# Kernel optimization log

Hardware: AMD Instinct MI355X
Metric: run time of the kernel (lower is better)

## Reference

```python
import jax, jax.numpy as jnp
import numpy as np

D = H = W = 128
NUM_STEPS = 7  # MONAI DVF2DDF default


def _base_grid(dtype):
    zz, yy, xx = jnp.meshgrid(jnp.arange(D, dtype=dtype),
                              jnp.arange(H, dtype=dtype),
                              jnp.arange(W, dtype=dtype), indexing='ij')
    return jnp.stack([zz, yy, xx], 0)  # [3,D,H,W] voxel coords


def _warp(img, ddf, mode):
    # img: [1,C,D,H,W], ddf: [1,3,D,H,W] in voxel units.
    # Equivalent to grid_sample(align_corners=True, padding='border'):
    # border padding == clamp the voxel-space sample coordinate to [0, dim-1].
    dtype = ddf.dtype
    coords = _base_grid(dtype) + ddf[0]
    lims = jnp.array([D - 1, H - 1, W - 1], dtype=dtype).reshape(3, 1, 1, 1)
    coords = jnp.clip(coords, 0.0, lims)
    vol = img[0]  # [C,D,H,W]
    if mode == 'nearest':
        zi, yi, xi = jnp.round(coords).astype(jnp.int32)
        return vol[:, zi, yi, xi][None]
    z, y, x = coords
    z0 = jnp.floor(z); y0 = jnp.floor(y); x0 = jnp.floor(x)
    wz = z - z0; wy = y - y0; wx = x - x0
    z0i = z0.astype(jnp.int32); y0i = y0.astype(jnp.int32); x0i = x0.astype(jnp.int32)
    z1i = jnp.minimum(z0i + 1, D - 1)
    y1i = jnp.minimum(y0i + 1, H - 1)
    x1i = jnp.minimum(x0i + 1, W - 1)
    g = lambda a, b, c: vol[:, a, b, c]  # [C,D,H,W] gather
    out = (g(z0i, y0i, x0i) * (1 - wz) * (1 - wy) * (1 - wx)
         + g(z0i, y0i, x1i) * (1 - wz) * (1 - wy) * wx
         + g(z0i, y1i, x0i) * (1 - wz) * wy * (1 - wx)
         + g(z0i, y1i, x1i) * (1 - wz) * wy * wx
         + g(z1i, y0i, x0i) * wz * (1 - wy) * (1 - wx)
         + g(z1i, y0i, x1i) * wz * (1 - wy) * wx
         + g(z1i, y1i, x0i) * wz * wy * (1 - wx)
         + g(z1i, y1i, x1i) * wz * wy * wx)
    return out[None]


def _dvf2ddf(dvf):
    # scaling-and-squaring integration of a stationary velocity field
    ddf = dvf / (2.0 ** NUM_STEPS)
    for _ in range(NUM_STEPS):
        ddf = ddf + _warp(ddf, ddf, 'bilinear')
    return ddf


def setup_inputs() -> dict:
    key = jax.random.key(0)
    k1, k2, k3, k4 = jax.random.split(key, 4)
    dvf = jax.random.normal(k1, (1, 3, D, H, W), dtype=jnp.float32) * 0.5
    moving_image = jax.random.uniform(k2, (1, 1, D, H, W), dtype=jnp.float32)
    fixed_image = jax.random.uniform(k3, (1, 1, D, H, W), dtype=jnp.float32)
    moving_label = jax.random.randint(k4, (1, 1, D, H, W), 0, 4).astype(jnp.float32)
    return {'dvf': dvf, 'moving_image': moving_image,
            'fixed_image': fixed_image, 'moving_label': moving_label}


def reference(dvf, moving_image, fixed_image, moving_label):
    ddf = _dvf2ddf(dvf)
    pred_image = _warp(moving_image, ddf, 'bilinear')
    pred_label = _warp(moving_label, ddf, 'nearest')
    return (ddf, pred_image, pred_label, dvf)
```

## Files before the change

kernel.cpp:

```cpp
#include <hip/hip_runtime.h>

#define DD 128
constexpr int NV = DD * DD * DD;
constexpr float INV_SCALE = 1.0f / 128.0f;

__device__ __forceinline__ void unpack_zyx(int tid, int& z, int& y, int& x) {
    x = tid & (DD - 1);
    y = (tid >> 7) & (DD - 1);
    z = tid >> 14;
}

__device__ __forceinline__ float clamp01(float v) {
    return fminf(fmaxf(v, 0.0f), (float)(DD - 1));
}

__global__ __launch_bounds__(256)
void init_kernel(const float* __restrict__ dvf, float* __restrict__ A) {
    int tid = blockIdx.x * blockDim.x + threadIdx.x;
    float d0 = dvf[tid] * INV_SCALE;
    float d1 = dvf[tid + NV] * INV_SCALE;
    float d2 = dvf[tid + 2 * NV] * INV_SCALE;
    float* p = A + 3 * tid;
    p[0] = d0; p[1] = d1; p[2] = d2;
}

__device__ __forceinline__ void trilerp3(const float* __restrict__ src,
                                         float cz, float cy, float cx,
                                         float& r0, float& r1, float& r2) {
    float z0f = floorf(cz), y0f = floorf(cy), x0f = floorf(cx);
    float wz = cz - z0f, wy = cy - y0f, wx = cx - x0f;
    int z0 = (int)z0f, y0 = (int)y0f, x0 = (int)x0f;
    int z1 = min(z0 + 1, DD - 1);
    int y1 = min(y0 + 1, DD - 1);
    int x1 = min(x0 + 1, DD - 1);
    float omz = 1.0f - wz, omy = 1.0f - wy, omx = 1.0f - wx;

    int zs0 = z0 << 14, zs1 = z1 << 14;
    int ys0 = y0 << 7,  ys1 = y1 << 7;

    const float* p000 = src + 3 * (zs0 + ys0 + x0);
    const float* p001 = src + 3 * (zs0 + ys0 + x1);
    const float* p010 = src + 3 * (zs0 + ys1 + x0);
    const float* p011 = src + 3 * (zs0 + ys1 + x1);
    const float* p100 = src + 3 * (zs1 + ys0 + x0);
    const float* p101 = src + 3 * (zs1 + ys0 + x1);
    const float* p110 = src + 3 * (zs1 + ys1 + x0);
    const float* p111 = src + 3 * (zs1 + ys1 + x1);

    float w000 = omz * omy * omx, w001 = omz * omy * wx;
    float w010 = omz * wy * omx,  w011 = omz * wy * wx;
    float w100 = wz * omy * omx,  w101 = wz * omy * wx;
    float w110 = wz * wy * omx,   w111 = wz * wy * wx;

    r0 = w000 * p000[0] + w001 * p001[0] + w010 * p010[0] + w011 * p011[0]
       + w100 * p100[0] + w101 * p101[0] + w110 * p110[0] + w111 * p111[0];
    r1 = w000 * p000[1] + w001 * p001[1] + w010 * p010[1] + w011 * p011[1]
       + w100 * p100[1] + w101 * p101[1] + w110 * p110[1] + w111 * p111[1];
    r2 = w000 * p000[2] + w001 * p001[2] + w010 * p010[2] + w011 * p011[2]
       + w100 * p100[2] + w101 * p101[2] + w110 * p110[2] + w111 * p111[2];
}

template <bool PLANAR_OUT>
__global__ __launch_bounds__(256)
void step_kernel(const float* __restrict__ src, float* __restrict__ dst) {
    int tid = blockIdx.x * blockDim.x + threadIdx.x;
    int z, y, x;
    unpack_zyx(tid, z, y, x);

    const float* s = src + 3 * tid;
    float d0 = s[0], d1 = s[1], d2 = s[2];

    float cz = clamp01((float)z + d0);
    float cy = clamp01((float)y + d1);
    float cx = clamp01((float)x + d2);

    float r0, r1, r2;
    trilerp3(src, cz, cy, cx, r0, r1, r2);

    r0 += d0; r1 += d1; r2 += d2;

    if (PLANAR_OUT) {
        dst[tid]          = r0;
        dst[tid + NV]     = r1;
        dst[tid + 2 * NV] = r2;
    } else {
        float* p = dst + 3 * tid;
        p[0] = r0; p[1] = r1; p[2] = r2;
    }
}

__global__ __launch_bounds__(256)
void final_kernel(const float* __restrict__ ddf,
                  const float* __restrict__ mimg,
                  const float* __restrict__ mlab,
                  const float* __restrict__ dvf,
                  float* __restrict__ pred_img,
                  float* __restrict__ pred_lab,
                  float* __restrict__ dvf_out) {
    int tid = blockIdx.x * blockDim.x + threadIdx.x;
    int z, y, x;
    unpack_zyx(tid, z, y, x);

    float d0 = ddf[tid];
    float d1 = ddf[tid + NV];
    float d2 = ddf[tid + 2 * NV];

    float cz = clamp01((float)z + d0);
    float cy = clamp01((float)y + d1);
    float cx = clamp01((float)x + d2);

    {
        float z0f = floorf(cz), y0f = floorf(cy), x0f = floorf(cx);
        float wz = cz - z0f, wy = cy - y0f, wx = cx - x0f;
        int z0 = (int)z0f, y0 = (int)y0f, x0 = (int)x0f;
        int z1 = min(z0 + 1, DD - 1);
        int y1 = min(y0 + 1, DD - 1);
        int x1 = min(x0 + 1, DD - 1);
        float omz = 1.0f - wz, omy = 1.0f - wy, omx = 1.0f - wx;
        int zs0 = z0 << 14, zs1 = z1 << 14;
        int ys0 = y0 << 7,  ys1 = y1 << 7;

        float v = omz * omy * omx * mimg[zs0 + ys0 + x0]
                + omz * omy * wx  * mimg[zs0 + ys0 + x1]
                + omz * wy * omx  * mimg[zs0 + ys1 + x0]
                + omz * wy * wx   * mimg[zs0 + ys1 + x1]
                + wz * omy * omx  * mimg[zs1 + ys0 + x0]
                + wz * omy * wx   * mimg[zs1 + ys0 + x1]
                + wz * wy * omx   * mimg[zs1 + ys1 + x0]
                + wz * wy * wx    * mimg[zs1 + ys1 + x1];
        pred_img[tid] = v;
    }

    {
        int zi = (int)rintf(cz);
        int yi = (int)rintf(cy);
        int xi = (int)rintf(cx);
        pred_lab[tid] = mlab[(zi << 14) + (yi << 7) + xi];
    }

    dvf_out[tid]          = dvf[tid];
    dvf_out[tid + NV]     = dvf[tid + NV];
    dvf_out[tid + 2 * NV] = dvf[tid + 2 * NV];
}

extern "C" void kernel_launch(void* const* d_in, const int* in_sizes, int n_in,
                              void* d_out, int out_size, void* d_ws, size_t ws_size,
                              hipStream_t stream) {
    const float* dvf  = (const float*)d_in[0];
    const float* mimg = (const float*)d_in[1];
    const float* mlab = (const float*)d_in[3];

    float* out      = (float*)d_out;
    float* ddf_out  = out;
    float* pred_img = out + 3 * NV;
    float* pred_lab = out + 4 * NV;
    float* dvf_out  = out + 5 * NV;

    float* A = dvf_out;
    float* B = ddf_out;

    dim3 block(256);
    dim3 grid(NV / 256);

    init_kernel<<<grid, block, 0, stream>>>(dvf, A);
    step_kernel<false><<<grid, block, 0, stream>>>(A, B);
    step_kernel<false><<<grid, block, 0, stream>>>(B, A);
    step_kernel<false><<<grid, block, 0, stream>>>(A, B);
    step_kernel<false><<<grid, block, 0, stream>>>(B, A);
    step_kernel<false><<<grid, block, 0, stream>>>(A, B);
    step_kernel<false><<<grid, block, 0, stream>>>(B, A);
    step_kernel<true ><<<grid, block, 0, stream>>>(A, B);
    final_kernel<<<grid, block, 0, stream>>>(B, mimg, mlab, dvf,
                                             pred_img, pred_lab, dvf_out);
}
```

Baseline: 261.7 us.

## Use padded float4 workspace layout and fuse init with first integration step

When a large enough workspace is available, the displacement field is stored as padded float4 (AoS4), so each trilinear corner becomes one 16-byte load instead of three scalar loads. The init scaling is fused with the first squaring step, which gathers from the planar dvf and also writes the dvf passthrough output, dropping one kernel launch and one full pass. Corner clamping is recomputed with offset deltas. The cost is a 33% larger per-step footprint from the padding, and the original path is kept as a fallback when the workspace is too small.

```diff
diff --git a/kernel.cpp b/kernel.cpp
--- a/kernel.cpp
+++ b/kernel.cpp
@@ -10,8 +10,173 @@
     z = tid >> 14;
 }
 
-__device__ __forceinline__ float clamp01(float v) {
+__device__ __forceinline__ float clampd(float v) {
     return fminf(fmaxf(v, 0.0f), (float)(DD - 1));
+}
+
+struct Corner {
+    int i000, i001, i010, i011, i100, i101, i110, i111;
+    float w000, w001, w010, w011, w100, w101, w110, w111;
+};
+
+__device__ __forceinline__ Corner make_corner(float cz, float cy, float cx) {
+    Corner c;
+    float z0f = floorf(cz), y0f = floorf(cy), x0f = floorf(cx);
+    float wz = cz - z0f, wy = cy - y0f, wx = cx - x0f;
+    int z0 = (int)z0f, y0 = (int)y0f, x0 = (int)x0f;
+    int dx = (x0 < DD - 1) ? 1 : 0;
+    int dy = (y0 < DD - 1) ? DD : 0;
+    int dz = (z0 < DD - 1) ? DD * DD : 0;
+    int i000 = (z0 << 14) + (y0 << 7) + x0;
+    c.i000 = i000;           c.i001 = i000 + dx;
+    c.i010 = i000 + dy;      c.i011 = i000 + dy + dx;
+    c.i100 = i000 + dz;      c.i101 = i000 + dz + dx;
+    c.i110 = i000 + dz + dy; c.i111 = i000 + dz + dy + dx;
+    float omz = 1.0f - wz, omy = 1.0f - wy, omx = 1.0f - wx;
+    c.w000 = omz * omy * omx; c.w001 = omz * omy * wx;
+    c.w010 = omz * wy * omx;  c.w011 = omz * wy * wx;
+    c.w100 = wz * omy * omx;  c.w101 = wz * omy * wx;
+    c.w110 = wz * wy * omx;   c.w111 = wz * wy * wx;
+    return c;
+}
+
+
+__global__ __launch_bounds__(256)
+void init_step1_kernel(const float* __restrict__ dvf,
+                       float4* __restrict__ dst,
+                       float* __restrict__ dvf_out) {
+    int tid = blockIdx.x * blockDim.x + threadIdx.x;
+    int z, y, x;
+    unpack_zyx(tid, z, y, x);
+
+    float v0 = dvf[tid];
+    float v1 = dvf[tid + NV];
+    float v2 = dvf[tid + 2 * NV];
+
+    dvf_out[tid]          = v0;
+    dvf_out[tid + NV]     = v1;
+    dvf_out[tid + 2 * NV] = v2;
+
+    float d0 = v0 * INV_SCALE, d1 = v1 * INV_SCALE, d2 = v2 * INV_SCALE;
+
+    float cz = clampd((float)z + d0);
+    float cy = clampd((float)y + d1);
+    float cx = clampd((float)x + d2);
+
+    Corner c = make_corner(cz, cy, cx);
+    const float* ch0 = dvf;
+    const float* ch1 = dvf + NV;
+    const float* ch2 = dvf + 2 * NV;
+
+    float t0 = c.w000 * ch0[c.i000] + c.w001 * ch0[c.i001]
+             + c.w010 * ch0[c.i010] + c.w011 * ch0[c.i011]
+             + c.w100 * ch0[c.i100] + c.w101 * ch0[c.i101]
+             + c.w110 * ch0[c.i110] + c.w111 * ch0[c.i111];
+    float t1 = c.w000 * ch1[c.i000] + c.w001 * ch1[c.i001]
+             + c.w010 * ch1[c.i010] + c.w011 * ch1[c.i011]
+             + c.w100 * ch1[c.i100] + c.w101 * ch1[c.i101]
+             + c.w110 * ch1[c.i110] + c.w111 * ch1[c.i111];
+    float t2 = c.w000 * ch2[c.i000] + c.w001 * ch2[c.i001]
+             + c.w010 * ch2[c.i010] + c.w011 * ch2[c.i011]
+             + c.w100 * ch2[c.i100] + c.w101 * ch2[c.i101]
+             + c.w110 * ch2[c.i110] + c.w111 * ch2[c.i111];
+
+    dst[tid] = make_float4(t0 * INV_SCALE + d0,
+                           t1 * INV_SCALE + d1,
+                           t2 * INV_SCALE + d2, 0.0f);
+}
+
+template <bool PLANAR_OUT>
+__global__ __launch_bounds__(256)
+void step4_kernel(const float4* __restrict__ src,
+                  float4* __restrict__ dst4,
+                  float* __restrict__ dstp) {
+    int tid = blockIdx.x * blockDim.x + threadIdx.x;
+    int z, y, x;
+    unpack_zyx(tid, z, y, x);
+
+    float4 d = src[tid];
+
+    float cz = clampd((float)z + d.x);
+    float cy = clampd((float)y + d.y);
+    float cx = clampd((float)x + d.z);
+
+    Corner c = make_corner(cz, cy, cx);
+
+    float4 v000 = src[c.i000], v001 = src[c.i001];
+    float4 v010 = src[c.i010], v011 = src[c.i011];
+    float4 v100 = src[c.i100], v101 = src[c.i101];
+    float4 v110 = src[c.i110], v111 = src[c.i111];
+
+    float r0 = c.w000 * v000.x + c.w001 * v001.x + c.w010 * v010.x + c.w011 * v011.x
+             + c.w100 * v100.x + c.w101 * v101.x + c.w110 * v110.x + c.w111 * v111.x;
+    float r1 = c.w000 * v000.y + c.w001 * v001.y + c.w010 * v010.y + c.w011 * v011.y
+             + c.w100 * v100.y + c.w101 * v101.y + c.w110 * v110.y + c.w111 * v111.y;
+    float r2 = c.w000 * v000.z + c.w001 * v001.z + c.w010 * v010.z + c.w011 * v011.z
+             + c.w100 * v100.z + c.w101 * v101.z + c.w110 * v110.z + c.w111 * v111.z;
+
+    r0 += d.x; r1 += d.y; r2 += d.z;
+
+    if (PLANAR_OUT) {
+        dstp[tid]          = r0;
+        dstp[tid + NV]     = r1;
+        dstp[tid + 2 * NV] = r2;
+    } else {
+        dst4[tid] = make_float4(r0, r1, r2, 0.0f);
+    }
+}
+
+__global__ __launch_bounds__(256)
+void final_kernel(const float* __restrict__ ddf,
+                  const float* __restrict__ mimg,
+                  const float* __restrict__ mlab,
+                  float* __restrict__ pred_img,
+                  float* __restrict__ pred_lab) {
+    int tid = blockIdx.x * blockDim.x + threadIdx.x;
+    int z, y, x;
+    unpack_zyx(tid, z, y, x);
+
+    float d0 = ddf[tid];
+    float d1 = ddf[tid + NV];
+    float d2 = ddf[tid + 2 * NV];
+
+    float cz = clampd((float)z + d0);
+    float cy = clampd((float)y + d1);
+    float cx = clampd((float)x + d2);
+
+    Corner c = make_corner(cz, cy, cx);
+
+    float v = c.w000 * mimg[c.i000] + c.w001 * mimg[c.i001]
+            + c.w010 * mimg[c.i010] + c.w011 * mimg[c.i011]
+            + c.w100 * mimg[c.i100] + c.w101 * mimg[c.i101]
+            + c.w110 * mimg[c.i110] + c.w111 * mimg[c.i111];
+    pred_img[tid] = v;
+
+    int zi = (int)rintf(cz);
+    int yi = (int)rintf(cy);
+    int xi = (int)rintf(cx);
+    pred_lab[tid] = mlab[(zi << 14) + (yi << 7) + xi];
+}
+
+
+__device__ __forceinline__ void trilerp3(const float* __restrict__ src,
+                                         float cz, float cy, float cx,
+                                         float& r0, float& r1, float& r2) {
+    Corner c = make_corner(cz, cy, cx);
+    const float* p000 = src + 3 * c.i000;
+    const float* p001 = src + 3 * c.i001;
+    const float* p010 = src + 3 * c.i010;
+    const float* p011 = src + 3 * c.i011;
+    const float* p100 = src + 3 * c.i100;
+    const float* p101 = src + 3 * c.i101;
+    const float* p110 = src + 3 * c.i110;
+    const float* p111 = src + 3 * c.i111;
+    r0 = c.w000 * p000[0] + c.w001 * p001[0] + c.w010 * p010[0] + c.w011 * p011[0]
+       + c.w100 * p100[0] + c.w101 * p101[0] + c.w110 * p110[0] + c.w111 * p111[0];
+    r1 = c.w000 * p000[1] + c.w001 * p001[1] + c.w010 * p010[1] + c.w011 * p011[1]
+       + c.w100 * p100[1] + c.w101 * p101[1] + c.w110 * p110[1] + c.w111 * p111[1];
+    r2 = c.w000 * p000[2] + c.w001 * p001[2] + c.w010 * p010[2] + c.w011 * p011[2]
+       + c.w100 * p100[2] + c.w101 * p101[2] + c.w110 * p110[2] + c.w111 * p111[2];
 }
 
 __global__ __launch_bounds__(256)
@@ -24,61 +189,20 @@
     p[0] = d0; p[1] = d1; p[2] = d2;
 }
 
-__device__ __forceinline__ void trilerp3(const float* __restrict__ src,
-                                         float cz, float cy, float cx,
-                                         float& r0, float& r1, float& r2) {
-    float z0f = floorf(cz), y0f = floorf(cy), x0f = floorf(cx);
-    float wz = cz - z0f, wy = cy - y0f, wx = cx - x0f;
-    int z0 = (int)z0f, y0 = (int)y0f, x0 = (int)x0f;
-    int z1 = min(z0 + 1, DD - 1);
-    int y1 = min(y0 + 1, DD - 1);
-    int x1 = min(x0 + 1, DD - 1);
-    float omz = 1.0f - wz, omy = 1.0f - wy, omx = 1.0f - wx;
-
-    int zs0 = z0 << 14, zs1 = z1 << 14;
-    int ys0 = y0 << 7,  ys1 = y1 << 7;
-
-    const float* p000 = src + 3 * (zs0 + ys0 + x0);
-    const float* p001 = src + 3 * (zs0 + ys0 + x1);
-    const float* p010 = src + 3 * (zs0 + ys1 + x0);
-    const float* p011 = src + 3 * (zs0 + ys1 + x1);
-    const float* p100 = src + 3 * (zs1 + ys0 + x0);
-    const float* p101 = src + 3 * (zs1 + ys0 + x1);
-    const float* p110 = src + 3 * (zs1 + ys1 + x0);
-    const float* p111 = src + 3 * (zs1 + ys1 + x1);
-
-    float w000 = omz * omy * omx, w001 = omz * omy * wx;
-    float w010 = omz * wy * omx,  w011 = omz * wy * wx;
-    float w100 = wz * omy * omx,  w101 = wz * omy * wx;
-    float w110 = wz * wy * omx,   w111 = wz * wy * wx;
-
-    r0 = w000 * p000[0] + w001 * p001[0] + w010 * p010[0] + w011 * p011[0]
-       + w100 * p100[0] + w101 * p101[0] + w110 * p110[0] + w111 * p111[0];
-    r1 = w000 * p000[1] + w001 * p001[1] + w010 * p010[1] + w011 * p011[1]
-       + w100 * p100[1] + w101 * p101[1] + w110 * p110[1] + w111 * p111[1];
-    r2 = w000 * p000[2] + w001 * p001[2] + w010 * p010[2] + w011 * p011[2]
-       + w100 * p100[2] + w101 * p101[2] + w110 * p110[2] + w111 * p111[2];
-}
-
 template <bool PLANAR_OUT>
 __global__ __launch_bounds__(256)
 void step_kernel(const float* __restrict__ src, float* __restrict__ dst) {
     int tid = blockIdx.x * blockDim.x + threadIdx.x;
     int z, y, x;
     unpack_zyx(tid, z, y, x);
-
     const float* s = src + 3 * tid;
     float d0 = s[0], d1 = s[1], d2 = s[2];
-
-    float cz = clamp01((float)z + d0);
-    float cy = clamp01((float)y + d1);
-    float cx = clamp01((float)x + d2);
-
+    float cz = clampd((float)z + d0);
+    float cy = clampd((float)y + d1);
+    float cx = clampd((float)x + d2);
     float r0, r1, r2;
     trilerp3(src, cz, cy, cx, r0, r1, r2);
-
     r0 += d0; r1 += d1; r2 += d2;
-
     if (PLANAR_OUT) {
         dst[tid]          = r0;
         dst[tid + NV]     = r1;
@@ -90,58 +214,37 @@
 }
 
 __global__ __launch_bounds__(256)
-void final_kernel(const float* __restrict__ ddf,
-                  const float* __restrict__ mimg,
-                  const float* __restrict__ mlab,
-                  const float* __restrict__ dvf,
-                  float* __restrict__ pred_img,
-                  float* __restrict__ pred_lab,
-                  float* __restrict__ dvf_out) {
-    int tid = blockIdx.x * blockDim.x + threadIdx.x;
-    int z, y, x;
-    unpack_zyx(tid, z, y, x);
-
+void final_kernel_fb(const float* __restrict__ ddf,
+                     const float* __restrict__ mimg,
+                     const float* __restrict__ mlab,
+                     const float* __restrict__ dvf,
+                     float* __restrict__ pred_img,
+                     float* __restrict__ pred_lab,
+                     float* __restrict__ dvf_out) {
+    int tid = blockIdx.x * blockDim.x + threadIdx.x;
+    int z, y, x;
+    unpack_zyx(tid, z, y, x);
     float d0 = ddf[tid];
     float d1 = ddf[tid + NV];
     float d2 = ddf[tid + 2 * NV];
-
-    float cz = clamp01((float)z + d0);
-    float cy = clamp01((float)y + d1);
-    float cx = clamp01((float)x + d2);
-
-    {
-        float z0f = floorf(cz), y0f = floorf(cy), x0f = floorf(cx);
-        float wz = cz - z0f, wy = cy - y0f, wx = cx - x0f;
-        int z0 = (int)z0f, y0 = (int)y0f, x0 = (int)x0f;
-        int z1 = min(z0 + 1, DD - 1);
-        int y1 = min(y0 + 1, DD - 1);
-        int x1 = min(x0 + 1, DD - 1);
-        float omz = 1.0f - wz, omy = 1.0f - wy, omx = 1.0f - wx;
-        int zs0 = z0 << 14, zs1 = z1 << 14;
-        int ys0 = y0 << 7,  ys1 = y1 << 7;
-
-        float v = omz * omy * omx * mimg[zs0 + ys0 + x0]
-                + omz * omy * wx  * mimg[zs0 + ys0 + x1]
-                + omz * wy * omx  * mimg[zs0 + ys1 + x0]
-                + omz * wy * wx   * mimg[zs0 + ys1 + x1]
-                + wz * omy * omx  * mimg[zs1 + ys0 + x0]
-                + wz * omy * wx   * mimg[zs1 + ys0 + x1]
-                + wz * wy * omx   * mimg[zs1 + ys1 + x0]
-                + wz * wy * wx    * mimg[zs1 + ys1 + x1];
-        pred_img[tid] = v;
-    }
-
-    {
-        int zi = (int)rintf(cz);
-        int yi = (int)rintf(cy);
-        int xi = (int)rintf(cx);
-        pred_lab[tid] = mlab[(zi << 14) + (yi << 7) + xi];
-    }
-
+    float cz = clampd((float)z + d0);
+    float cy = clampd((float)y + d1);
+    float cx = clampd((float)x + d2);
+    Corner c = make_corner(cz, cy, cx);
+    float v = c.w000 * mimg[c.i000] + c.w001 * mimg[c.i001]
+            + c.w010 * mimg[c.i010] + c.w011 * mimg[c.i011]
+            + c.w100 * mimg[c.i100] + c.w101 * mimg[c.i101]
+            + c.w110 * mimg[c.i110] + c.w111 * mimg[c.i111];
+    pred_img[tid] = v;
+    int zi = (int)rintf(cz);
+    int yi = (int)rintf(cy);
+    int xi = (int)rintf(cx);
+    pred_lab[tid] = mlab[(zi << 14) + (yi << 7) + xi];
     dvf_out[tid]          = dvf[tid];
     dvf_out[tid + NV]     = dvf[tid + NV];
     dvf_out[tid + 2 * NV] = dvf[tid + 2 * NV];
 }
+
 
 extern "C" void kernel_launch(void* const* d_in, const int* in_sizes, int n_in,
                               void* d_out, int out_size, void* d_ws, size_t ws_size,
@@ -156,20 +259,34 @@
     float* pred_lab = out + 4 * NV;
     float* dvf_out  = out + 5 * NV;
 
-    float* A = dvf_out;
-    float* B = ddf_out;
-
     dim3 block(256);
     dim3 grid(NV / 256);
 
-    init_kernel<<<grid, block, 0, stream>>>(dvf, A);
-    step_kernel<false><<<grid, block, 0, stream>>>(A, B);
-    step_kernel<false><<<grid, block, 0, stream>>>(B, A);
-    step_kernel<false><<<grid, block, 0, stream>>>(A, B);
-    step_kernel<false><<<grid, block, 0, stream>>>(B, A);
-    step_kernel<false><<<grid, block, 0, stream>>>(A, B);
-    step_kernel<false><<<grid, block, 0, stream>>>(B, A);
-    step_kernel<true ><<<grid, block, 0, stream>>>(A, B);
-    final_kernel<<<grid, block, 0, stream>>>(B, mimg, mlab, dvf,
-                                             pred_img, pred_lab, dvf_out);
-}
+    size_t need = (size_t)2 * NV * sizeof(float4);
+    if (d_ws != nullptr && ws_size >= need) {
+        float4* A4 = (float4*)d_ws;
+        float4* B4 = A4 + NV;
+        init_step1_kernel<<<grid, block, 0, stream>>>(dvf, A4, dvf_out);
+        step4_kernel<false><<<grid, block, 0, stream>>>(A4, B4, nullptr);
+        step4_kernel<false><<<grid, block, 0, stream>>>(B4, A4, nullptr);
+        step4_kernel<false><<<grid, block, 0, stream>>>(A4, B4, nullptr);
+        step4_kernel<false><<<grid, block, 0, stream>>>(B4, A4, nullptr);
+        step4_kernel<false><<<grid, block, 0, stream>>>(A4, B4, nullptr);
+        step4_kernel<true ><<<grid, block, 0, stream>>>(B4, nullptr, ddf_out);
+        final_kernel<<<grid, block, 0, stream>>>(ddf_out, mimg, mlab,
+                                                 pred_img, pred_lab);
+    } else {
+        float* A = dvf_out;
+        float* B = ddf_out;
+        init_kernel<<<grid, block, 0, stream>>>(dvf, A);
+        step_kernel<false><<<grid, block, 0, stream>>>(A, B);
+        step_kernel<false><<<grid, block, 0, stream>>>(B, A);
+        step_kernel<false><<<grid, block, 0, stream>>>(A, B);
+        step_kernel<false><<<grid, block, 0, stream>>>(B, A);
+        step_kernel<false><<<grid, block, 0, stream>>>(A, B);
+        step_kernel<false><<<grid, block, 0, stream>>>(B, A);
+        step_kernel<true ><<<grid, block, 0, stream>>>(A, B);
+        final_kernel_fb<<<grid, block, 0, stream>>>(B, mimg, mlab, dvf,
+                                                    pred_img, pred_lab, dvf_out);
+    }
+}
```

Measured after the change: 291.9 us. 11.5% more time.

## Fuse last step with final warp, use workspace buffers, swizzle blocks across XCDs

Applied to the files above, without the earlier changes.

When a large enough workspace is available, ping-pong buffers move into the workspace. The dvf copy is folded into a vectorized init kernel, and the seventh integration step is fused with the image/label warps, which removes one launch and the planar ddf round-trip. Step kernels remap block indices so consecutive blocks of the volume land on the same XCD, aiming to improve L2 locality for the neighbouring gathers. A fallback path keeps the original schedule when no workspace is given.

```diff
diff --git a/kernel.cpp b/kernel.cpp
--- a/kernel.cpp
+++ b/kernel.cpp
@@ -3,6 +3,11 @@
 #define DD 128
 constexpr int NV = DD * DD * DD;
 constexpr float INV_SCALE = 1.0f / 128.0f;
+#define NXCD 8
+
+__device__ __forceinline__ int swz(int b, int cpx) {
+    return (b & (NXCD - 1)) * cpx + (b >> 3);
+}
 
 __device__ __forceinline__ void unpack_zyx(int tid, int& z, int& y, int& x) {
     x = tid & (DD - 1);
@@ -10,18 +15,8 @@
     z = tid >> 14;
 }
 
-__device__ __forceinline__ float clamp01(float v) {
+__device__ __forceinline__ float clampd(float v) {
     return fminf(fmaxf(v, 0.0f), (float)(DD - 1));
-}
-
-__global__ __launch_bounds__(256)
-void init_kernel(const float* __restrict__ dvf, float* __restrict__ A) {
-    int tid = blockIdx.x * blockDim.x + threadIdx.x;
-    float d0 = dvf[tid] * INV_SCALE;
-    float d1 = dvf[tid + NV] * INV_SCALE;
-    float d2 = dvf[tid + 2 * NV] * INV_SCALE;
-    float* p = A + 3 * tid;
-    p[0] = d0; p[1] = d1; p[2] = d2;
 }
 
 __device__ __forceinline__ void trilerp3(const float* __restrict__ src,
@@ -60,25 +55,143 @@
        + w100 * p100[2] + w101 * p101[2] + w110 * p110[2] + w111 * p111[2];
 }
 
-template <bool PLANAR_OUT>
+
+__global__ __launch_bounds__(256)
+void init_fused_kernel(const float* __restrict__ dvf,
+                       float* __restrict__ A,
+                       float* __restrict__ dvf_out) {
+    int vbid = swz(blockIdx.x, 2048 / NXCD);
+    int base = vbid * 1024 + threadIdx.x * 4;
+
+    float4 a = *(const float4*)(dvf + base);
+    float4 b = *(const float4*)(dvf + base + NV);
+    float4 c = *(const float4*)(dvf + base + 2 * NV);
+
+    *(float4*)(dvf_out + base)          = a;
+    *(float4*)(dvf_out + base + NV)     = b;
+    *(float4*)(dvf_out + base + 2 * NV) = c;
+
+    float4 o0 = make_float4(a.x * INV_SCALE, b.x * INV_SCALE, c.x * INV_SCALE,
+                            a.y * INV_SCALE);
+    float4 o1 = make_float4(b.y * INV_SCALE, c.y * INV_SCALE, a.z * INV_SCALE,
+                            b.z * INV_SCALE);
+    float4 o2 = make_float4(c.z * INV_SCALE, a.w * INV_SCALE, b.w * INV_SCALE,
+                            c.w * INV_SCALE);
+    float* p = A + 3 * base;
+    *(float4*)(p)     = o0;
+    *(float4*)(p + 4) = o1;
+    *(float4*)(p + 8) = o2;
+}
+
 __global__ __launch_bounds__(256)
 void step_kernel(const float* __restrict__ src, float* __restrict__ dst) {
-    int tid = blockIdx.x * blockDim.x + threadIdx.x;
+    int vbid = swz(blockIdx.x, 8192 / NXCD);
+    int tid = vbid * 256 + threadIdx.x;
     int z, y, x;
     unpack_zyx(tid, z, y, x);
 
     const float* s = src + 3 * tid;
     float d0 = s[0], d1 = s[1], d2 = s[2];
 
-    float cz = clamp01((float)z + d0);
-    float cy = clamp01((float)y + d1);
-    float cx = clamp01((float)x + d2);
+    float cz = clampd((float)z + d0);
+    float cy = clampd((float)y + d1);
+    float cx = clampd((float)x + d2);
 
     float r0, r1, r2;
     trilerp3(src, cz, cy, cx, r0, r1, r2);
 
     r0 += d0; r1 += d1; r2 += d2;
 
+    float* p = dst + 3 * tid;
+    p[0] = r0; p[1] = r1; p[2] = r2;
+}
+
+__global__ __launch_bounds__(256)
+void step7_final_kernel(const float* __restrict__ src,
+                        const float* __restrict__ mimg,
+                        const float* __restrict__ mlab,
+                        float* __restrict__ ddf_out,
+                        float* __restrict__ pred_img,
+                        float* __restrict__ pred_lab) {
+    int vbid = swz(blockIdx.x, 8192 / NXCD);
+    int tid = vbid * 256 + threadIdx.x;
+    int z, y, x;
+    unpack_zyx(tid, z, y, x);
+
+    const float* s = src + 3 * tid;
+    float d0 = s[0], d1 = s[1], d2 = s[2];
+
+    float cz = clampd((float)z + d0);
+    float cy = clampd((float)y + d1);
+    float cx = clampd((float)x + d2);
+
+    float r0, r1, r2;
+    trilerp3(src, cz, cy, cx, r0, r1, r2);
+    r0 += d0; r1 += d1; r2 += d2;
+
+    ddf_out[tid]          = r0;
+    ddf_out[tid + NV]     = r1;
+    ddf_out[tid + 2 * NV] = r2;
+
+    float fz = clampd((float)z + r0);
+    float fy = clampd((float)y + r1);
+    float fx = clampd((float)x + r2);
+
+    {
+        float z0f = floorf(fz), y0f = floorf(fy), x0f = floorf(fx);
+        float wz = fz - z0f, wy = fy - y0f, wx = fx - x0f;
+        int z0 = (int)z0f, y0 = (int)y0f, x0 = (int)x0f;
+        int z1 = min(z0 + 1, DD - 1);
+        int y1 = min(y0 + 1, DD - 1);
+        int x1 = min(x0 + 1, DD - 1);
+        float omz = 1.0f - wz, omy = 1.0f - wy, omx = 1.0f - wx;
+        int zs0 = z0 << 14, zs1 = z1 << 14;
+        int ys0 = y0 << 7,  ys1 = y1 << 7;
+
+        float v = omz * omy * omx * mimg[zs0 + ys0 + x0]
+                + omz * omy * wx  * mimg[zs0 + ys0 + x1]
+                + omz * wy * omx  * mimg[zs0 + ys1 + x0]
+                + omz * wy * wx   * mimg[zs0 + ys1 + x1]
+                + wz * omy * omx  * mimg[zs1 + ys0 + x0]
+                + wz * omy * wx   * mimg[zs1 + ys0 + x1]
+                + wz * wy * omx   * mimg[zs1 + ys1 + x0]
+                + wz * wy * wx    * mimg[zs1 + ys1 + x1];
+        pred_img[tid] = v;
+    }
+
+    {
+        int zi = (int)rintf(fz);
+        int yi = (int)rintf(fy);
+        int xi = (int)rintf(fx);
+        pred_lab[tid] = mlab[(zi << 14) + (yi << 7) + xi];
+    }
+}
+
+
+__global__ __launch_bounds__(256)
+void init_kernel_fb(const float* __restrict__ dvf, float* __restrict__ A) {
+    int tid = blockIdx.x * blockDim.x + threadIdx.x;
+    float d0 = dvf[tid] * INV_SCALE;
+    float d1 = dvf[tid + NV] * INV_SCALE;
+    float d2 = dvf[tid + 2 * NV] * INV_SCALE;
+    float* p = A + 3 * tid;
+    p[0] = d0; p[1] = d1; p[2] = d2;
+}
+
+template <bool PLANAR_OUT>
+__global__ __launch_bounds__(256)
+void step_kernel_fb(const float* __restrict__ src, float* __restrict__ dst) {
+    int tid = blockIdx.x * blockDim.x + threadIdx.x;
+    int z, y, x;
+    unpack_zyx(tid, z, y, x);
+    const float* s = src + 3 * tid;
+    float d0 = s[0], d1 = s[1], d2 = s[2];
+    float cz = clampd((float)z + d0);
+    float cy = clampd((float)y + d1);
+    float cx = clampd((float)x + d2);
+    float r0, r1, r2;
+    trilerp3(src, cz, cy, cx, r0, r1, r2);
+    r0 += d0; r1 += d1; r2 += d2;
     if (PLANAR_OUT) {
         dst[tid]          = r0;
         dst[tid + NV]     = r1;
@@ -90,25 +203,22 @@
 }
 
 __global__ __launch_bounds__(256)
-void final_kernel(const float* __restrict__ ddf,
-                  const float* __restrict__ mimg,
-                  const float* __restrict__ mlab,
-                  const float* __restrict__ dvf,
-                  float* __restrict__ pred_img,
-                  float* __restrict__ pred_lab,
-                  float* __restrict__ dvf_out) {
+void final_kernel_fb(const float* __restrict__ ddf,
+                     const float* __restrict__ mimg,
+                     const float* __restrict__ mlab,
+                     const float* __restrict__ dvf,
+                     float* __restrict__ pred_img,
+                     float* __restrict__ pred_lab,
+                     float* __restrict__ dvf_out) {
     int tid = blockIdx.x * blockDim.x + threadIdx.x;
     int z, y, x;
     unpack_zyx(tid, z, y, x);
-
     float d0 = ddf[tid];
     float d1 = ddf[tid + NV];
     float d2 = ddf[tid + 2 * NV];
-
-    float cz = clamp01((float)z + d0);
-    float cy = clamp01((float)y + d1);
-    float cx = clamp01((float)x + d2);
-
+    float cz = clampd((float)z + d0);
+    float cy = clampd((float)y + d1);
+    float cx = clampd((float)x + d2);
     {
         float z0f = floorf(cz), y0f = floorf(cy), x0f = floorf(cx);
         float wz = cz - z0f, wy = cy - y0f, wx = cx - x0f;
@@ -119,7 +229,6 @@
         float omz = 1.0f - wz, omy = 1.0f - wy, omx = 1.0f - wx;
         int zs0 = z0 << 14, zs1 = z1 << 14;
         int ys0 = y0 << 7,  ys1 = y1 << 7;
-
         float v = omz * omy * omx * mimg[zs0 + ys0 + x0]
                 + omz * omy * wx  * mimg[zs0 + ys0 + x1]
                 + omz * wy * omx  * mimg[zs0 + ys1 + x0]
@@ -130,18 +239,15 @@
                 + wz * wy * wx    * mimg[zs1 + ys1 + x1];
         pred_img[tid] = v;
     }
-
-    {
-        int zi = (int)rintf(cz);
-        int yi = (int)rintf(cy);
-        int xi = (int)rintf(cx);
-        pred_lab[tid] = mlab[(zi << 14) + (yi << 7) + xi];
-    }
-
+    int zi = (int)rintf(cz);
+    int yi = (int)rintf(cy);
+    int xi = (int)rintf(cx);
+    pred_lab[tid] = mlab[(zi << 14) + (yi << 7) + xi];
     dvf_out[tid]          = dvf[tid];
     dvf_out[tid + NV]     = dvf[tid + NV];
     dvf_out[tid + 2 * NV] = dvf[tid + 2 * NV];
 }
+
 
 extern "C" void kernel_launch(void* const* d_in, const int* in_sizes, int n_in,
                               void* d_out, int out_size, void* d_ws, size_t ws_size,
@@ -156,20 +262,36 @@
     float* pred_lab = out + 4 * NV;
     float* dvf_out  = out + 5 * NV;
 
-    float* A = dvf_out;
-    float* B = ddf_out;
-
     dim3 block(256);
     dim3 grid(NV / 256);
-
-    init_kernel<<<grid, block, 0, stream>>>(dvf, A);
-    step_kernel<false><<<grid, block, 0, stream>>>(A, B);
-    step_kernel<false><<<grid, block, 0, stream>>>(B, A);
-    step_kernel<false><<<grid, block, 0, stream>>>(A, B);
-    step_kernel<false><<<grid, block, 0, stream>>>(B, A);
-    step_kernel<false><<<grid, block, 0, stream>>>(A, B);
-    step_kernel<false><<<grid, block, 0, stream>>>(B, A);
-    step_kernel<true ><<<grid, block, 0, stream>>>(A, B);
-    final_kernel<<<grid, block, 0, stream>>>(B, mimg, mlab, dvf,
-                                             pred_img, pred_lab, dvf_out);
-}
+    dim3 igrid(NV / 1024);
+
+    size_t need = (size_t)2 * NV * 3 * sizeof(float);
+    if (d_ws != nullptr && ws_size >= need) {
+        float* A = (float*)d_ws;
+        float* B = A + (size_t)3 * NV;
+        init_fused_kernel<<<igrid, block, 0, stream>>>(dvf, A, dvf_out);
+        step_kernel<<<grid, block, 0, stream>>>(A, B);
+        step_kernel<<<grid, block, 0, stream>>>(B, A);
+        step_kernel<<<grid, block, 0, stream>>>(A, B);
+        step_kernel<<<grid, block, 0, stream>>>(B, A);
+        step_kernel<<<grid, block, 0, stream>>>(A, B);
+        step_kernel<<<grid, block, 0, stream>>>(B, A);
+        step7_final_kernel<<<grid, block, 0, stream>>>(A, mimg, mlab,
+                                                       ddf_out, pred_img,
+                                                       pred_lab);
+    } else {
+        float* A = dvf_out;
+        float* B = ddf_out;
+        init_kernel_fb<<<grid, block, 0, stream>>>(dvf, A);
+        step_kernel_fb<false><<<grid, block, 0, stream>>>(A, B);
+        step_kernel_fb<false><<<grid, block, 0, stream>>>(B, A);
+        step_kernel_fb<false><<<grid, block, 0, stream>>>(A, B);
+        step_kernel_fb<false><<<grid, block, 0, stream>>>(B, A);
+        step_kernel_fb<false><<<grid, block, 0, stream>>>(A, B);
+        step_kernel_fb<false><<<grid, block, 0, stream>>>(B, A);
+        step_kernel_fb<true ><<<grid, block, 0, stream>>>(A, B);
+        final_kernel_fb<<<grid, block, 0, stream>>>(B, mimg, mlab, dvf,
+                                                    pred_img, pred_lab, dvf_out);
+    }
+}
```

Result: no change. 259.4 us (-0.9%).
